# Optimization experiments

Measured on AMD Instinct MI355X. Metric: run time of the kernel, lower is better.

Reference implementation:

```python
import jax, jax.numpy as jnp
import numpy as np

B, S, D = 2, 2048, 2048
H, HK, HD = 16, 4, 128          # query heads, kv heads, head dim (H*HD == D)
HID = 4 * D                      # SwiGLU hidden (mult=4)
WIN, SINK = 1024, 4              # sliding window, attention sink tokens
EPS = 1e-6
ROPE_BASE = 10000.0


def rmsnorm(x, g):
    return x * jax.lax.rsqrt(jnp.mean(x * x, axis=-1, keepdims=True) + EPS) * g


def rope_tables(seq_len, head_dim):
    inv = 1.0 / (ROPE_BASE ** (jnp.arange(0, head_dim, 2, dtype=jnp.float32) / head_dim))
    ang = jnp.arange(seq_len, dtype=jnp.float32)[:, None] * inv[None, :]  # [S, HD/2]
    return jnp.cos(ang), jnp.sin(ang)


def apply_rope(x, cos, sin):
    # x: [B, S, h, HD]; rotate-half convention
    x1, x2 = jnp.split(x, 2, axis=-1)
    c = cos[None, :, None, :]
    s = sin[None, :, None, :]
    return jnp.concatenate([x1 * c - x2 * s, x2 * c + x1 * s], axis=-1)


def setup_inputs() -> dict:
    key = jax.random.key(0)
    ks = jax.random.split(key, 10)
    p = 0.02
    return {
        "x": jax.random.normal(ks[0], (B, S, D), dtype=jnp.float32),
        "g1": jnp.ones((D,), dtype=jnp.float32),
        "g2": jnp.ones((D,), dtype=jnp.float32),
        "wq": jax.random.normal(ks[1], (D, H * HD), dtype=jnp.float32) * p,
        "wk": jax.random.normal(ks[2], (D, HK * HD), dtype=jnp.float32) * p,
        "wv": jax.random.normal(ks[3], (D, HK * HD), dtype=jnp.float32) * p,
        "wo": jax.random.normal(ks[4], (H * HD, D), dtype=jnp.float32) * p,
        "w_gate": jax.random.normal(ks[5], (D, HID), dtype=jnp.float32) * p,
        "w_up": jax.random.normal(ks[6], (D, HID), dtype=jnp.float32) * p,
        "w_down": jax.random.normal(ks[7], (HID, D), dtype=jnp.float32) * p,
    }


def reference(x, g1, g2, wq, wk, wv, wo, w_gate, w_up, w_down):
    # ---- pre-norm attention ----
    h = rmsnorm(x, g1)
    q = (h @ wq).reshape(B, S, H, HD)
    k = (h @ wk).reshape(B, S, HK, HD)
    v = (h @ wv).reshape(B, S, HK, HD)

    cos, sin = rope_tables(S, HD)
    q = apply_rope(q, cos, sin)
    k = apply_rope(k, cos, sin)

    # GQA: expand kv heads to query heads
    rep = H // HK
    k = jnp.repeat(k, rep, axis=2)  # [B, S, H, HD]
    v = jnp.repeat(v, rep, axis=2)

    scores = jnp.einsum("bqhd,bkhd->bhqk", q, k) / jnp.sqrt(jnp.float32(HD))

    # causal + sliding-window + attention-sink mask
    i = jnp.arange(S)[:, None]
    j = jnp.arange(S)[None, :]
    allowed = (j <= i) & (((i - j) < WIN) | (j < SINK))  # [S, S]
    scores = jnp.where(allowed[None, None], scores, jnp.float32(-1e9))

    attn = jax.nn.softmax(scores, axis=-1)
    a = jnp.einsum("bhqk,bkhd->bqhd", attn, v).reshape(B, S, H * HD) @ wo

    x = x + a

    # ---- pre-norm SwiGLU FFN ----
    h2 = rmsnorm(x, g2)
    ffn = (jax.nn.silu(h2 @ w_gate) * (h2 @ w_up)) @ w_down
    return x + ffn
```

## Files before the change

kernel.cpp:

```cpp
#include <hip/hip_runtime.h>
#include <hip/hip_bf16.h>
#include <stdint.h>

#define TOK 4096
#define SEQ 2048
#define DM 2048
#define NH 16
#define NKV 4
#define HDIM 128
#define HID 8192
#define WIN 1024
#define SINKN 4

typedef float f32x4 __attribute__((ext_vector_type(4)));
typedef __bf16 bf16x8 __attribute__((ext_vector_type(8)));
typedef unsigned short u16;
typedef unsigned int u32;

#define VM(n) asm volatile("s_waitcnt vmcnt(" #n ")" ::: "memory")
#define LG(n) asm volatile("s_waitcnt lgkmcnt(" #n ")" ::: "memory")
#define SCHED0 __builtin_amdgcn_sched_barrier(0)

__device__ __forceinline__ u16 f2bf(float f) {
  union { float f; u32 u; } v; v.f = f;
  return (u16)((v.u + 0x7fffu + ((v.u >> 16) & 1u)) >> 16);
}
__device__ __forceinline__ float bf2f(u16 h) {
  union { u32 u; float f; } v; v.u = ((u32)h) << 16;
  return v.f;
}
__device__ __forceinline__ f32x4 mfma16(bf16x8 a, bf16x8 b, f32x4 c) {
  return __builtin_amdgcn_mfma_f32_16x16x32_bf16(a, b, c, 0, 0, 0);
}
__device__ __forceinline__ void gld16(const u16* g, u16* l) {
  __builtin_amdgcn_global_load_lds(
      (const __attribute__((address_space(1))) u32*)g,
      (__attribute__((address_space(3))) u32*)l, 16, 0, 0);
}
__device__ __forceinline__ void bar() {
  asm volatile("s_barrier" ::: "memory");
}
__device__ __forceinline__ void swz_rc(int c, int& row, int& k8) {
  row = 2 * (c >> 3) + (((c >> 2) & 1) ^ ((c >> 4) & 1));
  k8 = (c & 3) ^ (row & 3);
}
__device__ __forceinline__ void raster8(int wg, int nwg, int nbx, int& bx, int& by) {
  int cpx = nwg >> 3;
  int s = (wg & 7) * cpx + (wg >> 3);
  by = 8 * (s / (8 * nbx)) + (s & 7);
  bx = (s >> 3) % nbx;
}

__global__ __launch_bounds__(256)
void wtrans(const float* __restrict__ in, u16* __restrict__ out, int K, int N)
{
  __shared__ float t[32][33];
  int tx = threadIdx.x & 31, ty = threadIdx.x >> 5;
  int bx = blockIdx.x, by = blockIdx.y;
  #pragma unroll
  for (int i = 0; i < 4; i++) {
    int r = ty + i * 8;
    t[r][tx] = in[(size_t)(by * 32 + r) * N + bx * 32 + tx];
  }
  __syncthreads();
  #pragma unroll
  for (int i = 0; i < 4; i++) {
    int r = ty + i * 8;
    out[(size_t)(bx * 32 + r) * K + by * 32 + tx] = f2bf(t[tx][r]);
  }
}

__global__ __launch_bounds__(256)
void vtrans(const u16* __restrict__ in, int ld, u16* __restrict__ out)
{
  __shared__ u16 t[32][33];
  int tx = threadIdx.x & 31, ty = threadIdx.x >> 5;
  int bx = blockIdx.x;
  int by = blockIdx.y;
  #pragma unroll
  for (int i = 0; i < 4; i++) {
    int r = ty + i * 8;
    t[r][tx] = in[(size_t)(by * 32 + r) * ld + bx * 32 + tx];
  }
  __syncthreads();
  int b = (by * 32) >> 11;
  int s0 = (by * 32) & (SEQ - 1);
  #pragma unroll
  for (int i = 0; i < 4; i++) {
    int c = bx * 32 + ty + i * 8;
    out[(size_t)(b * (NKV * HDIM) + c) * SEQ + s0 + tx] = t[tx][ty + i * 8];
  }
}

__global__ __launch_bounds__(256)
void rope_table_k(float* __restrict__ ct, float* __restrict__ st)
{
  int idx = blockIdx.x * 256 + threadIdx.x;
  int pos = idx >> 6, d = idx & 63;
  float inv = powf(10000.0f, -(float)d / 64.0f);
  float a = (float)pos * inv;
  ct[idx] = cosf(a);
  st[idx] = sinf(a);
}

__global__ void rope_apply_k(u16* __restrict__ q, int ld,
                             const float* __restrict__ ct,
                             const float* __restrict__ st, float scale)
{
  int t = blockIdx.x;
  int hh = threadIdx.x >> 6;
  int d = threadIdx.x & 63;
  int pos = t & (SEQ - 1);
  size_t base = (size_t)t * ld + hh * HDIM + d;
  float x1 = bf2f(q[base]), x2 = bf2f(q[base + 64]);
  float c = ct[pos * 64 + d], s = st[pos * 64 + d];
  q[base]      = f2bf((x1 * c - x2 * s) * scale);
  q[base + 64] = f2bf((x2 * c + x1 * s) * scale);
}

__global__ __launch_bounds__(256)
void rmsnorm_k(const float* __restrict__ x, const float* __restrict__ g,
               u16* __restrict__ o)
{
  int row = blockIdx.x;
  int tid = threadIdx.x;
  const float* xr = x + (size_t)row * DM;
  float4 v0 = *(const float4*)(xr + tid * 8);
  float4 v1 = *(const float4*)(xr + tid * 8 + 4);
  float ss = v0.x*v0.x + v0.y*v0.y + v0.z*v0.z + v0.w*v0.w
           + v1.x*v1.x + v1.y*v1.y + v1.z*v1.z + v1.w*v1.w;
  #pragma unroll
  for (int d = 1; d < 64; d <<= 1) ss += __shfl_xor(ss, d);
  __shared__ float red[4];
  if ((tid & 63) == 0) red[tid >> 6] = ss;
  __syncthreads();
  float inv = rsqrtf((red[0] + red[1] + red[2] + red[3]) * (1.0f / DM) + 1e-6f);
  float4 g0 = *(const float4*)(g + tid * 8);
  float4 g1 = *(const float4*)(g + tid * 8 + 4);
  ushort4 o0, o1;
  o0.x = f2bf(v0.x * inv * g0.x); o0.y = f2bf(v0.y * inv * g0.y);
  o0.z = f2bf(v0.z * inv * g0.z); o0.w = f2bf(v0.w * inv * g0.w);
  o1.x = f2bf(v1.x * inv * g1.x); o1.y = f2bf(v1.y * inv * g1.y);
  o1.z = f2bf(v1.z * inv * g1.z); o1.w = f2bf(v1.w * inv * g1.w);
  *(ushort4*)(o + (size_t)row * DM + tid * 8) = o0;
  *(ushort4*)(o + (size_t)row * DM + tid * 8 + 4) = o1;
}

template<int EPI>
__global__ __launch_bounds__(512, 1)
void gemmp(const u16* __restrict__ A, const u16* __restrict__ Bt,
           u16* __restrict__ Cb, float* __restrict__ Cf,
           const float* __restrict__ X, int M, int N, int K, int nbx)
{
  constexpr int ASZ = 128 * 64;
  constexpr int SLOT = ASZ + 256 * 64;
  __shared__ u16 lds[3 * SLOT];

  int bx, by;
  raster8(blockIdx.x, gridDim.x, nbx, bx, by);
  int m0 = by * 128;
  int n0 = bx * 256;

  int tid = threadIdx.x;
  int l = tid & 63, w = tid >> 6;
  int l16 = l & 15, lg = l >> 4;
  int wr = w >> 2, wc = w & 3;

  int aoff[4][2], boff[4][2];
  #pragma unroll
  for (int m = 0; m < 4; m++)
    #pragma unroll
    for (int kk = 0; kk < 2; kk++) {
      int row = wr * 64 + m * 16 + l16;
      aoff[m][kk] = ((row * 128 + kk * 64 + lg * 16) ^ ((row & 7) << 4)) >> 1;
    }
  #pragma unroll
  for (int n = 0; n < 4; n++)
    #pragma unroll
    for (int kk = 0; kk < 2; kk++) {
      int br = wc * 64 + n * 16 + l16;
      boff[n][kk] = ASZ + (((br * 128 + kk * 64 + lg * 16) ^ ((br & 7) << 4)) >> 1);
    }

  int urow = tid >> 3;
  int cc = (tid & 7) ^ (urow & 7);
  const u16* pA[2];
  const u16* pB[4];
  pA[0] = A + (size_t)(m0 + urow) * K + cc * 8;
  pA[1] = A + (size_t)(m0 + 64 + urow) * K + cc * 8;
  #pragma unroll
  for (int u = 0; u < 4; u++)
    pB[u] = Bt + (size_t)(n0 + u * 64 + urow) * K + cc * 8;

  const int NT = K >> 6;

  auto stA = [&](int tt, int u) {
    gld16(pA[u] + (size_t)tt * 64, lds + (tt % 3) * SLOT + u * 4096 + tid * 8);
  };
  auto stB = [&](int tt, int u) {
    gld16(pB[u] + (size_t)tt * 64, lds + (tt % 3) * SLOT + ASZ + u * 4096 + tid * 8);
  };

  #pragma unroll
  for (int u = 0; u < 4; u++) stB(0, u);
  stA(0, 0); stA(0, 1);
  #pragma unroll
  for (int u = 0; u < 4; u++) stB(1, u);
  stA(1, 0); stA(1, 1);
  VM(6);
  bar();

  f32x4 acc[4][4];
  f32x4 zero = {0.f, 0.f, 0.f, 0.f};
  #pragma unroll
  for (int m = 0; m < 4; m++)
    #pragma unroll
    for (int n = 0; n < 4; n++) acc[m][n] = zero;

  for (int t = 0; t < NT; ++t) {
    u16* cur = lds + (t % 3) * SLOT;
    const bool st = (t + 2 < NT);

    if (st) { stB(t + 2, 0); stB(t + 2, 1); stB(t + 2, 2); }
    bf16x8 a[4][2], b[2][2], c2[2][2];
    #pragma unroll
    for (int m = 0; m < 4; m++) {
      a[m][0] = *(const bf16x8*)(cur + aoff[m][0]);
      a[m][1] = *(const bf16x8*)(cur + aoff[m][1]);
    }
    #pragma unroll
    for (int n = 0; n < 2; n++) {
      b[n][0] = *(const bf16x8*)(cur + boff[n][0]);
      b[n][1] = *(const bf16x8*)(cur + boff[n][1]);
    }
    SCHED0;
    #pragma unroll
    for (int n = 0; n < 2; n++) {
      c2[n][0] = *(const bf16x8*)(cur + boff[n + 2][0]);
      c2[n][1] = *(const bf16x8*)(cur + boff[n + 2][1]);
    }
    bar();
    LG(4);
    SCHED0;
    __builtin_amdgcn_s_setprio(1);
    #pragma unroll
    for (int m = 0; m < 4; m++)
      #pragma unroll
      for (int n = 0; n < 2; n++) {
        acc[m][n] = mfma16(a[m][0], b[n][0], acc[m][n]);
        acc[m][n] = mfma16(a[m][1], b[n][1], acc[m][n]);
      }
    __builtin_amdgcn_s_setprio(0);
    SCHED0;
    bar();

    if (st) { stB(t + 2, 3); stA(t + 2, 0); stA(t + 2, 1); }
    if (st) { VM(6); }
    else if (t + 1 < NT) { VM(0); }
    bar();
    LG(0);
    SCHED0;
    __builtin_amdgcn_s_setprio(1);
    #pragma unroll
    for (int m = 0; m < 4; m++)
      #pragma unroll
      for (int n = 0; n < 2; n++) {
        acc[m][n + 2] = mfma16(a[m][0], c2[n][0], acc[m][n + 2]);
        acc[m][n + 2] = mfma16(a[m][1], c2[n][1], acc[m][n + 2]);
      }
    __builtin_amdgcn_s_setprio(0);
    SCHED0;
    bar();
  }

  #pragma unroll
  for (int m = 0; m < 4; m++) {
    int row = m0 + wr * 64 + m * 16 + lg * 4;
    #pragma unroll
    for (int n = 0; n < 4; n++) {
      int col = n0 + wc * 64 + n * 16 + l16;
      #pragma unroll
      for (int r = 0; r < 4; r++) {
        size_t idx = (size_t)(row + r) * N + col;
        float v = acc[m][n][r];
        if (EPI == 0) {
          Cb[idx] = f2bf(v);
        } else if (EPI == 1) {
          Cf[idx] = X[idx] + v;
        } else {
          Cf[idx] += v;
        }
      }
    }
  }
}

template<int EPI, int GU, int SPLITK>
__global__ __launch_bounds__(512, 1)
void gemm256(const u16* __restrict__ A, const u16* __restrict__ B1,
             const u16* __restrict__ B2, u16* __restrict__ Cb,
             float* __restrict__ Cf, int Kst, int NT, int N, int nbx)
{
  constexpr int SLOT = 32768;
  __shared__ u16 lds[2 * SLOT];

  int wg = blockIdx.x;
  int nwg = gridDim.x;
  int kh = 0;
  if (SPLITK) { int half = nwg >> 1; kh = (wg >= half); wg -= kh * half; nwg = half; }
  int bx, by;
  raster8(wg, nwg, nbx, bx, by);
  int m0 = by * 256;
  int n0 = bx * (GU ? 128 : 256);
  size_t k0 = (size_t)kh * NT * 64;

  int tid = threadIdx.x;
  int l = tid & 63, w = tid >> 6;
  int l16 = l & 15, lg = l >> 4;
  int wr = w >> 2, wc = w & 3;

  int aoff[4][2], boff[2][2];
  #pragma unroll
  for (int mm = 0; mm < 4; mm++)
    #pragma unroll
    for (int kk = 0; kk < 2; kk++) {
      int ar = wr * 64 + mm * 16 + l16;
      aoff[mm][kk] = ((ar * 128 + ((kk * 64 + lg * 16) ^ ((ar & 7) << 4))) >> 1);
    }
  #pragma unroll
  for (int nn = 0; nn < 2; nn++)
    #pragma unroll
    for (int kk = 0; kk < 2; kk++) {
      int br = wc * 32 + nn * 16 + l16;
      boff[nn][kk] = 16384 + ((br * 128 + ((kk * 64 + lg * 16) ^ ((br & 7) << 4))) >> 1);
    }

  int rh = tid >> 3;
  int cc = (tid & 7) ^ (rh & 7);
  const u16* pA[4];
  #pragma unroll
  for (int u = 0; u < 4; u++)
    pA[u] = A + (size_t)(m0 + u * 64 + rh) * Kst + k0 + cc * 8;
  const u16* pB[4];
  #pragma unroll
  for (int u = 0; u < 4; u++) {
    if (GU) pB[u] = (u < 2 ? B1 + (size_t)(n0 + u * 64 + rh) * Kst
                           : B2 + (size_t)(n0 + (u - 2) * 64 + rh) * Kst) + k0 + cc * 8;
    else    pB[u] = B1 + (size_t)(n0 + u * 64 + rh) * Kst + k0 + cc * 8;
  }

  auto stA = [&](int tt, int h) {
    u16* d = lds + (tt & 1) * SLOT + h * 8192;
    gld16(pA[h * 2 + 0] + (size_t)tt * 64, d + tid * 8);
    gld16(pA[h * 2 + 1] + (size_t)tt * 64, d + 4096 + tid * 8);
  };
  auto stB = [&](int tt, int h) {
    u16* d = lds + (tt & 1) * SLOT + 16384 + h * 8192;
    gld16(pB[h * 2 + 0] + (size_t)tt * 64, d + tid * 8);
    gld16(pB[h * 2 + 1] + (size_t)tt * 64, d + 4096 + tid * 8);
  };

  stA(0, 0); stB(0, 0); stA(0, 1); stB(0, 1);
  stA(1, 0); stB(1, 0); stA(1, 1);
  VM(6);
  bar();

  f32x4 acc[8][4];
  f32x4 zero = {0.f, 0.f, 0.f, 0.f};
  #pragma unroll
  for (int m = 0; m < 8; m++)
    #pragma unroll
    for (int n = 0; n < 4; n++) acc[m][n] = zero;

  for (int t = 0; t < NT; ++t) {
    u16* cur = lds + (t & 1) * SLOT;
    bf16x8 a0[4][2], a1[4][2], b0[2][2], b1[2][2];

    #pragma unroll
    for (int mm = 0; mm < 4; mm++)
      #pragma unroll
      for (int kk = 0; kk < 2; kk++)
        a0[mm][kk] = *(const bf16x8*)(cur + aoff[mm][kk]);
    #pragma unroll
    for (int nn = 0; nn < 2; nn++)
      #pragma unroll
      for (int kk = 0; kk < 2; kk++)
        b0[nn][kk] = *(const bf16x8*)(cur + boff[nn][kk]);
    if (t + 1 < NT) stB(t + 1, 1);
    LG(8);
    bar();
    LG(0);
    SCHED0;
    __builtin_amdgcn_s_setprio(1);
    #pragma unroll
    for (int mm = 0; mm < 4; mm++)
      #pragma unroll
      for (int nn = 0; nn < 2; nn++)
        #pragma unroll
        for (int kk = 0; kk < 2; kk++)
          acc[mm][nn] = mfma16(a0[mm][kk], b0[nn][kk], acc[mm][nn]);
    __builtin_amdgcn_s_setprio(0);
    SCHED0;
    bar();

    #pragma unroll
    for (int nn = 0; nn < 2; nn++)
      #pragma unroll
      for (int kk = 0; kk < 2; kk++)
        b1[nn][kk] = *(const bf16x8*)(cur + boff[nn][kk] + 8192);
    if (t + 2 < NT) stA(t + 2, 0);
    bar();
    LG(0);
    SCHED0;
    __builtin_amdgcn_s_setprio(1);
    #pragma unroll
    for (int mm = 0; mm < 4; mm++)
      #pragma unroll
      for (int nn = 0; nn < 2; nn++)
        #pragma unroll
        for (int kk = 0; kk < 2; kk++)
          acc[mm][2 + nn] = mfma16(a0[mm][kk], b1[nn][kk], acc[mm][2 + nn]);
    __builtin_amdgcn_s_setprio(0);
    SCHED0;
    bar();

    #pragma unroll
    for (int mm = 0; mm < 4; mm++)
      #pragma unroll
      for (int kk = 0; kk < 2; kk++)
        a1[mm][kk] = *(const bf16x8*)(cur + aoff[mm][kk] + 8192);
    if (t + 2 < NT) stB(t + 2, 0);
    bar();
    LG(0);
    SCHED0;
    __builtin_amdgcn_s_setprio(1);
    #pragma unroll
    for (int mm = 0; mm < 4; mm++)
      #pragma unroll
      for (int nn = 0; nn < 2; nn++)
        #pragma unroll
        for (int kk = 0; kk < 2; kk++)
          acc[4 + mm][nn] = mfma16(a1[mm][kk], b0[nn][kk], acc[4 + mm][nn]);
    __builtin_amdgcn_s_setprio(0);
    SCHED0;
    bar();

    if (t + 2 < NT) { stA(t + 2, 1); VM(6); }
    else if (t + 1 < NT) { VM(0); }
    bar();
    SCHED0;
    __builtin_amdgcn_s_setprio(1);
    #pragma unroll
    for (int mm = 0; mm < 4; mm++)
      #pragma unroll
      for (int nn = 0; nn < 2; nn++)
        #pragma unroll
        for (int kk = 0; kk < 2; kk++)
          acc[4 + mm][2 + nn] = mfma16(a1[mm][kk], b1[nn][kk], acc[4 + mm][2 + nn]);
    __builtin_amdgcn_s_setprio(0);
    SCHED0;
    bar();
  }

  if (GU) {
    #pragma unroll
    for (int m = 0; m < 8; m++) {
      int row = m0 + (m >> 2) * 128 + wr * 64 + (m & 3) * 16 + lg * 4;
      #pragma unroll
      for (int nn = 0; nn < 2; nn++) {
        int col = n0 + wc * 32 + nn * 16 + l16;
        #pragma unroll
        for (int r = 0; r < 4; r++) {
          float gt = acc[m][nn][r];
          float up = acc[m][2 + nn][r];
          float sg = gt / (1.0f + __expf(-gt));
          Cb[(size_t)(row + r) * N + col] = f2bf(sg * up);
        }
      }
    }
  } else {
    #pragma unroll
    for (int m = 0; m < 8; m++) {
      int row = m0 + (m >> 2) * 128 + wr * 64 + (m & 3) * 16 + lg * 4;
      #pragma unroll
      for (int n = 0; n < 4; n++) {
        int col = n0 + (n >> 1) * 128 + wc * 32 + (n & 1) * 16 + l16;
        #pragma unroll
        for (int r = 0; r < 4; r++) {
          size_t idx = (size_t)(row + r) * N + col;
          if (EPI == 0) Cb[idx] = f2bf(acc[m][n][r]);
          else          atomicAdd(Cf + idx, acc[m][n][r]);
        }
      }
    }
  }
}

__global__ __launch_bounds__(256)
void attn_k(const u16* __restrict__ qb, int ldq,
            const u16* __restrict__ kb, int ldk,
            const u16* __restrict__ vbt, u16* __restrict__ ao)
{
  int q0 = blockIdx.x * 128;
  int h = blockIdx.y;
  int b = blockIdx.z;
  int hk = h >> 2;
  int tid = threadIdx.x;
  int w = tid >> 6, l = tid & 63;
  int l16 = l & 15, lg = l >> 4;

  __shared__ u16 Ks[32 * 128];
  __shared__ u16 Vt[128 * 32];
  __shared__ u16 Ps[4][32 * 40];
  u16* Pw = Ps[w];

  bf16x8 qf[2][4];
  #pragma unroll
  for (int m = 0; m < 2; m++)
    #pragma unroll
    for (int kd = 0; kd < 4; kd++) {
      int row = q0 + w * 32 + m * 16 + l16;
      qf[m][kd] = *(const bf16x8*)(qb + (size_t)(b * SEQ + row) * ldq
                                   + h * HDIM + kd * 32 + lg * 8);
    }

  f32x4 oacc[2][8];
  float mrun[2][4], lrun[2][4];
  f32x4 zero = {0.f, 0.f, 0.f, 0.f};
  #pragma unroll
  for (int m = 0; m < 2; m++) {
    #pragma unroll
    for (int nd = 0; nd < 8; nd++) oacc[m][nd] = zero;
    #pragma unroll
    for (int r = 0; r < 4; r++) { mrun[m][r] = -1e9f; lrun[m][r] = 0.f; }
  }

  int kr0 = tid >> 4,        kc0 = (tid & 15) ^ (kr0 & 7);
  int kr1 = (tid + 256) >> 4, kc1 = (tid & 15) ^ (kr1 & 7);
  int vd0, vk0, vd1, vk1;
  swz_rc(tid, vd0, vk0);
  swz_rc(tid + 256, vd1, vk1);
  const u16* kbase = kb + (size_t)(b * SEQ) * ldk + hk * HDIM;
  const u16* vbase = vbt + (size_t)(b * NKV + hk) * HDIM * SEQ;

  int koff[2][4];
  #pragma unroll
  for (int n = 0; n < 2; n++)
    #pragma unroll
    for (int kd = 0; kd < 4; kd++) {
      int key = n * 16 + l16;
      koff[n][kd] = ((key * 128) + kd * 32 + lg * 8) ^ ((key & 7) * 8);
    }
  int voff[8];
  #pragma unroll
  for (int nd = 0; nd < 8; nd++) {
    int d = nd * 16 + l16;
    voff[nd] = (d * 32 + lg * 8) ^ ((d & 7) * 8);
  }

  int lo = (q0 >= WIN) ? ((q0 - (WIN - 1)) >> 5) : 0;
  int hi = (q0 + 127) >> 5;

  for (int it = (lo > 0 ? lo - 1 : 0); it <= hi; ++it) {
    int kt = (it < lo) ? 0 : it;
    gld16(kbase + (size_t)(kt * 32 + kr0) * ldk + kc0 * 8, Ks + tid * 8);
    gld16(kbase + (size_t)(kt * 32 + kr1) * ldk + kc1 * 8, Ks + (tid + 256) * 8);
    gld16(vbase + (size_t)vd0 * SEQ + kt * 32 + vk0 * 8, Vt + tid * 8);
    gld16(vbase + (size_t)vd1 * SEQ + kt * 32 + vk1 * 8, Vt + (tid + 256) * 8);
    __syncthreads();

    f32x4 sacc[2][2];
    sacc[0][0] = zero; sacc[0][1] = zero; sacc[1][0] = zero; sacc[1][1] = zero;
    #pragma unroll
    for (int kd = 0; kd < 4; kd++) {
      bf16x8 kf0 = *(const bf16x8*)(Ks + koff[0][kd]);
      bf16x8 kf1 = *(const bf16x8*)(Ks + koff[1][kd]);
      #pragma unroll
      for (int m = 0; m < 2; m++) {
        sacc[m][0] = mfma16(qf[m][kd], kf0, sacc[m][0]);
        sacc[m][1] = mfma16(qf[m][kd], kf1, sacc[m][1]);
      }
    }

    #pragma unroll
    for (int m = 0; m < 2; m++) {
      float sc[4];
      #pragma unroll
      for (int r = 0; r < 4; r++) {
        int i = q0 + w * 32 + m * 16 + lg * 4 + r;
        int j0 = kt * 32 + l16;
        int j1 = j0 + 16;
        float s0 = sacc[m][0][r];
        float s1 = sacc[m][1][r];
        bool ok0 = (j0 <= i) && ((i - j0 < WIN) || (j0 < SINKN));
        bool ok1 = (j1 <= i) && ((i - j1 < WIN) || (j1 < SINKN));
        s0 = ok0 ? s0 : -1e9f;
        s1 = ok1 ? s1 : -1e9f;
        float mx = fmaxf(s0, s1);
        mx = fmaxf(mx, __shfl_xor(mx, 1));
        mx = fmaxf(mx, __shfl_xor(mx, 2));
        mx = fmaxf(mx, __shfl_xor(mx, 4));
        mx = fmaxf(mx, __shfl_xor(mx, 8));
        float mold = mrun[m][r];
        float mnew = fmaxf(mold, mx);
        float scl = __expf(mold - mnew);
        mrun[m][r] = mnew;
        float p0 = __expf(s0 - mnew);
        float p1 = __expf(s1 - mnew);
        int prow = m * 16 + lg * 4 + r;
        Pw[prow * 40 + l16] = f2bf(p0);
        Pw[prow * 40 + 16 + l16] = f2bf(p1);
        float ps = p0 + p1;
        ps += __shfl_xor(ps, 1);
        ps += __shfl_xor(ps, 2);
        ps += __shfl_xor(ps, 4);
        ps += __shfl_xor(ps, 8);
        lrun[m][r] = lrun[m][r] * scl + ps;
        sc[r] = scl;
      }
      #pragma unroll
      for (int nd = 0; nd < 8; nd++) {
        oacc[m][nd][0] *= sc[0];
        oacc[m][nd][1] *= sc[1];
        oacc[m][nd][2] *= sc[2];
        oacc[m][nd][3] *= sc[3];
      }
    }

    bf16x8 pa0 = *(const bf16x8*)(Pw + l16 * 40 + lg * 8);
    bf16x8 pa1 = *(const bf16x8*)(Pw + (16 + l16) * 40 + lg * 8);
    #pragma unroll
    for (int nd = 0; nd < 8; nd++) {
      bf16x8 vf = *(const bf16x8*)(Vt + voff[nd]);
      oacc[0][nd] = mfma16(pa0, vf, oacc[0][nd]);
      oacc[1][nd] = mfma16(pa1, vf, oacc[1][nd]);
    }
    __syncthreads();
  }

  #pragma unroll
  for (int m = 0; m < 2; m++)
    #pragma unroll
    for (int r = 0; r < 4; r++) {
      float invl = 1.0f / lrun[m][r];
      int row = q0 + w * 32 + m * 16 + lg * 4 + r;
      #pragma unroll
      for (int nd = 0; nd < 8; nd++) {
        int col = nd * 16 + l16;
        ao[(size_t)(b * SEQ + row) * (NH * HDIM) + h * HDIM + col] =
            f2bf(oacc[m][nd][r] * invl);
      }
    }
}

extern "C" void kernel_launch(void* const* d_in, const int* in_sizes, int n_in,
                              void* d_out, int out_size, void* d_ws, size_t ws_size,
                              hipStream_t stream)
{
  (void)in_sizes; (void)n_in; (void)out_size;
  const float* x  = (const float*)d_in[0];
  const float* g1 = (const float*)d_in[1];
  const float* g2 = (const float*)d_in[2];
  const float* wq = (const float*)d_in[3];
  const float* wk = (const float*)d_in[4];
  const float* wv = (const float*)d_in[5];
  const float* wo = (const float*)d_in[6];
  const float* wg = (const float*)d_in[7];
  const float* wu = (const float*)d_in[8];
  const float* wd = (const float*)d_in[9];
  float* out = (float*)d_out;

  char* ws = (char*)d_ws;
  size_t off = 0;
  auto alloc = [&](size_t bytes) {
    char* p = ws + off;
    off += (bytes + 255) & ~(size_t)255;
    return p;
  };
  const int NQKV = 3072;
  u16* wqkv_t = (u16*)alloc((size_t)NQKV * DM * 2);
  u16* wo_t   = (u16*)alloc((size_t)DM * DM * 2);
  u16* wg_t   = (u16*)alloc((size_t)HID * DM * 2);
  u16* wu_t   = (u16*)alloc((size_t)HID * DM * 2);
  u16* wd_t   = (u16*)alloc((size_t)DM * HID * 2);
  u16* hb     = (u16*)alloc((size_t)TOK * DM * 2);
  char* span0 = ws + off;
  u16* qkvb   = (u16*)alloc((size_t)TOK * NQKV * 2);
  u16* vbt    = (u16*)alloc((size_t)TOK * NKV * HDIM * 2);
  u16* aob    = (u16*)alloc((size_t)TOK * NH * HDIM * 2);
  size_t span_used = (size_t)(ws + off - span0);
  size_t gu_need = (size_t)TOK * HID * 2;
  if (gu_need > span_used) alloc(gu_need - span_used);
  u16* gu = (u16*)span0;
  float* ct  = (float*)alloc((size_t)SEQ * 64 * 4);
  float* st  = (float*)alloc((size_t)SEQ * 64 * 4);
  if (off > ws_size) return;

  dim3 blk(256);
  dim3 blk512(512);

  wtrans<<<dim3(DM / 32, DM / 32), blk, 0, stream>>>(wq, wqkv_t, DM, DM);
  wtrans<<<dim3((NKV * HDIM) / 32, DM / 32), blk, 0, stream>>>(wk, wqkv_t + (size_t)DM * DM, DM, NKV * HDIM);
  wtrans<<<dim3((NKV * HDIM) / 32, DM / 32), blk, 0, stream>>>(wv, wqkv_t + (size_t)(DM + NKV * HDIM) * DM, DM, NKV * HDIM);
  wtrans<<<dim3(DM / 32, DM / 32), blk, 0, stream>>>(wo, wo_t, DM, DM);
  wtrans<<<dim3(HID / 32, DM / 32), blk, 0, stream>>>(wg, wg_t, DM, HID);
  wtrans<<<dim3(HID / 32, DM / 32), blk, 0, stream>>>(wu, wu_t, DM, HID);
  wtrans<<<dim3(DM / 32, HID / 32), blk, 0, stream>>>(wd, wd_t, HID, DM);

  rope_table_k<<<SEQ * 64 / 256, blk, 0, stream>>>(ct, st);
  rmsnorm_k<<<TOK, blk, 0, stream>>>(x, g1, hb);

  gemm256<0, 0, 0><<<dim3((NQKV / 256) * (TOK / 256)), blk512, 0, stream>>>(
      hb, wqkv_t, nullptr, qkvb, nullptr, DM, DM / 64, NQKV, NQKV / 256);

  rope_apply_k<<<TOK, dim3(NH * 64), 0, stream>>>(qkvb, NQKV, ct, st, 0.08838834764831845f);
  rope_apply_k<<<TOK, dim3(NKV * 64), 0, stream>>>(qkvb + DM, NQKV, ct, st, 1.0f);
  vtrans<<<dim3((NKV * HDIM) / 32, TOK / 32), blk, 0, stream>>>(qkvb + DM + NKV * HDIM, NQKV, vbt);

  attn_k<<<dim3(SEQ / 128, NH, 2), blk, 0, stream>>>(qkvb, NQKV, qkvb + DM, NQKV, vbt, aob);

  gemmp<1><<<dim3((DM / 256) * (TOK / 128)), blk512, 0, stream>>>(
      aob, wo_t, nullptr, out, x, TOK, DM, DM, DM / 256);
  rmsnorm_k<<<TOK, blk, 0, stream>>>(out, g2, hb);

  gemm256<0, 1, 0><<<dim3((HID / 128) * (TOK / 256)), blk512, 0, stream>>>(
      hb, wg_t, wu_t, gu, nullptr, DM, DM / 64, HID, HID / 128);

  gemm256<4, 0, 1><<<dim3(2 * (DM / 256) * (TOK / 256)), blk512, 0, stream>>>(
      gu, wd_t, nullptr, nullptr, out, HID, HID / 128, DM, DM / 256);
}
```

Before: 770.9 us.

## Merge weight transposes, double-buffer attention K/V, split-K the output projection

Merges the seven weight-transpose launches into one kernel that picks its source and destination from the block index. The attention kernel now double-buffers the K/V tiles with async loads, so the next tile's global load overlaps the current tile's compute. The output projection moves from the dedicated gemmp kernel to the split-K gemm256 path with an accumulate epilogue. The residual x is copied into out during the first rmsnorm so the split-K atomic adds accumulate onto it. It also adds unroll 2 to the gemm256 main loop, and the split-K accumulation order may make results nondeterministic.

```diff
diff --git a/kernel.cpp b/kernel.cpp
--- a/kernel.cpp
+++ b/kernel.cpp
@@ -52,21 +52,38 @@
 }
 
 __global__ __launch_bounds__(256)
-void wtrans(const float* __restrict__ in, u16* __restrict__ out, int K, int N)
-{
+void wtrans_all(const float* __restrict__ wq, const float* __restrict__ wk,
+                const float* __restrict__ wv, const float* __restrict__ wo,
+                const float* __restrict__ wg, const float* __restrict__ wu,
+                const float* __restrict__ wd,
+                u16* __restrict__ dqkv, u16* __restrict__ dwo,
+                u16* __restrict__ dwg, u16* __restrict__ dwu,
+                u16* __restrict__ dwd)
+{
+  int id = blockIdx.x;
+  const float* src; u16* dst; int K, N, lgn;
+  if (id < 4096)       { src = wq; dst = dqkv;                        K = 2048; N = 2048; lgn = 6; }
+  else if (id < 5120)  { id -= 4096;  src = wk; dst = dqkv + (size_t)DM * DM;          K = 2048; N = 512;  lgn = 4; }
+  else if (id < 6144)  { id -= 5120;  src = wv; dst = dqkv + (size_t)(DM + 512) * DM;  K = 2048; N = 512;  lgn = 4; }
+  else if (id < 10240) { id -= 6144;  src = wo; dst = dwo;            K = 2048; N = 2048; lgn = 6; }
+  else if (id < 26624) { id -= 10240; src = wg; dst = dwg;            K = 2048; N = 8192; lgn = 8; }
+  else if (id < 43008) { id -= 26624; src = wu; dst = dwu;            K = 2048; N = 8192; lgn = 8; }
+  else                 { id -= 43008; src = wd; dst = dwd;            K = 8192; N = 2048; lgn = 6; }
+  int bx = id & ((1 << lgn) - 1);
+  int by = id >> lgn;
+
   __shared__ float t[32][33];
   int tx = threadIdx.x & 31, ty = threadIdx.x >> 5;
-  int bx = blockIdx.x, by = blockIdx.y;
   #pragma unroll
   for (int i = 0; i < 4; i++) {
     int r = ty + i * 8;
-    t[r][tx] = in[(size_t)(by * 32 + r) * N + bx * 32 + tx];
+    t[r][tx] = src[(size_t)(by * 32 + r) * N + bx * 32 + tx];
   }
   __syncthreads();
   #pragma unroll
   for (int i = 0; i < 4; i++) {
     int r = ty + i * 8;
-    out[(size_t)(bx * 32 + r) * K + by * 32 + tx] = f2bf(t[tx][r]);
+    dst[(size_t)(bx * 32 + r) * K + by * 32 + tx] = f2bf(t[tx][r]);
   }
 }
 
@@ -120,7 +137,7 @@
 
 __global__ __launch_bounds__(256)
 void rmsnorm_k(const float* __restrict__ x, const float* __restrict__ g,
-               u16* __restrict__ o)
+               u16* __restrict__ o, float* __restrict__ xcopy)
 {
   int row = blockIdx.x;
   int tid = threadIdx.x;
@@ -135,6 +152,10 @@
   if ((tid & 63) == 0) red[tid >> 6] = ss;
   __syncthreads();
   float inv = rsqrtf((red[0] + red[1] + red[2] + red[3]) * (1.0f / DM) + 1e-6f);
+  if (xcopy) {
+    *(float4*)(xcopy + (size_t)row * DM + tid * 8) = v0;
+    *(float4*)(xcopy + (size_t)row * DM + tid * 8 + 4) = v1;
+  }
   float4 g0 = *(const float4*)(g + tid * 8);
   float4 g1 = *(const float4*)(g + tid * 8 + 4);
   ushort4 o0, o1;
@@ -144,155 +165,6 @@
   o1.z = f2bf(v1.z * inv * g1.z); o1.w = f2bf(v1.w * inv * g1.w);
   *(ushort4*)(o + (size_t)row * DM + tid * 8) = o0;
   *(ushort4*)(o + (size_t)row * DM + tid * 8 + 4) = o1;
-}
-
-template<int EPI>
-__global__ __launch_bounds__(512, 1)
-void gemmp(const u16* __restrict__ A, const u16* __restrict__ Bt,
-           u16* __restrict__ Cb, float* __restrict__ Cf,
-           const float* __restrict__ X, int M, int N, int K, int nbx)
-{
-  constexpr int ASZ = 128 * 64;
-  constexpr int SLOT = ASZ + 256 * 64;
-  __shared__ u16 lds[3 * SLOT];
-
-  int bx, by;
-  raster8(blockIdx.x, gridDim.x, nbx, bx, by);
-  int m0 = by * 128;
-  int n0 = bx * 256;
-
-  int tid = threadIdx.x;
-  int l = tid & 63, w = tid >> 6;
-  int l16 = l & 15, lg = l >> 4;
-  int wr = w >> 2, wc = w & 3;
-
-  int aoff[4][2], boff[4][2];
-  #pragma unroll
-  for (int m = 0; m < 4; m++)
-    #pragma unroll
-    for (int kk = 0; kk < 2; kk++) {
-      int row = wr * 64 + m * 16 + l16;
-      aoff[m][kk] = ((row * 128 + kk * 64 + lg * 16) ^ ((row & 7) << 4)) >> 1;
-    }
-  #pragma unroll
-  for (int n = 0; n < 4; n++)
-    #pragma unroll
-    for (int kk = 0; kk < 2; kk++) {
-      int br = wc * 64 + n * 16 + l16;
-      boff[n][kk] = ASZ + (((br * 128 + kk * 64 + lg * 16) ^ ((br & 7) << 4)) >> 1);
-    }
-
-  int urow = tid >> 3;
-  int cc = (tid & 7) ^ (urow & 7);
-  const u16* pA[2];
-  const u16* pB[4];
-  pA[0] = A + (size_t)(m0 + urow) * K + cc * 8;
-  pA[1] = A + (size_t)(m0 + 64 + urow) * K + cc * 8;
-  #pragma unroll
-  for (int u = 0; u < 4; u++)
-    pB[u] = Bt + (size_t)(n0 + u * 64 + urow) * K + cc * 8;
-
-  const int NT = K >> 6;
-
-  auto stA = [&](int tt, int u) {
-    gld16(pA[u] + (size_t)tt * 64, lds + (tt % 3) * SLOT + u * 4096 + tid * 8);
-  };
-  auto stB = [&](int tt, int u) {
-    gld16(pB[u] + (size_t)tt * 64, lds + (tt % 3) * SLOT + ASZ + u * 4096 + tid * 8);
-  };
-
-  #pragma unroll
-  for (int u = 0; u < 4; u++) stB(0, u);
-  stA(0, 0); stA(0, 1);
-  #pragma unroll
-  for (int u = 0; u < 4; u++) stB(1, u);
-  stA(1, 0); stA(1, 1);
-  VM(6);
-  bar();
-
-  f32x4 acc[4][4];
-  f32x4 zero = {0.f, 0.f, 0.f, 0.f};
-  #pragma unroll
-  for (int m = 0; m < 4; m++)
-    #pragma unroll
-    for (int n = 0; n < 4; n++) acc[m][n] = zero;
-
-  for (int t = 0; t < NT; ++t) {
-    u16* cur = lds + (t % 3) * SLOT;
-    const bool st = (t + 2 < NT);
-
-    if (st) { stB(t + 2, 0); stB(t + 2, 1); stB(t + 2, 2); }
-    bf16x8 a[4][2], b[2][2], c2[2][2];
-    #pragma unroll
-    for (int m = 0; m < 4; m++) {
-      a[m][0] = *(const bf16x8*)(cur + aoff[m][0]);
-      a[m][1] = *(const bf16x8*)(cur + aoff[m][1]);
-    }
-    #pragma unroll
-    for (int n = 0; n < 2; n++) {
-      b[n][0] = *(const bf16x8*)(cur + boff[n][0]);
-      b[n][1] = *(const bf16x8*)(cur + boff[n][1]);
-    }
-    SCHED0;
-    #pragma unroll
-    for (int n = 0; n < 2; n++) {
-      c2[n][0] = *(const bf16x8*)(cur + boff[n + 2][0]);
-      c2[n][1] = *(const bf16x8*)(cur + boff[n + 2][1]);
-    }
-    bar();
-    LG(4);
-    SCHED0;
-    __builtin_amdgcn_s_setprio(1);
-    #pragma unroll
-    for (int m = 0; m < 4; m++)
-      #pragma unroll
-      for (int n = 0; n < 2; n++) {
-        acc[m][n] = mfma16(a[m][0], b[n][0], acc[m][n]);
-        acc[m][n] = mfma16(a[m][1], b[n][1], acc[m][n]);
-      }
-    __builtin_amdgcn_s_setprio(0);
-    SCHED0;
-    bar();
-
-    if (st) { stB(t + 2, 3); stA(t + 2, 0); stA(t + 2, 1); }
-    if (st) { VM(6); }
-    else if (t + 1 < NT) { VM(0); }
-    bar();
-    LG(0);
-    SCHED0;
-    __builtin_amdgcn_s_setprio(1);
-    #pragma unroll
-    for (int m = 0; m < 4; m++)
-      #pragma unroll
-      for (int n = 0; n < 2; n++) {
-        acc[m][n + 2] = mfma16(a[m][0], c2[n][0], acc[m][n + 2]);
-        acc[m][n + 2] = mfma16(a[m][1], c2[n][1], acc[m][n + 2]);
-      }
-    __builtin_amdgcn_s_setprio(0);
-    SCHED0;
-    bar();
-  }
-
-  #pragma unroll
-  for (int m = 0; m < 4; m++) {
-    int row = m0 + wr * 64 + m * 16 + lg * 4;
-    #pragma unroll
-    for (int n = 0; n < 4; n++) {
-      int col = n0 + wc * 64 + n * 16 + l16;
-      #pragma unroll
-      for (int r = 0; r < 4; r++) {
-        size_t idx = (size_t)(row + r) * N + col;
-        float v = acc[m][n][r];
-        if (EPI == 0) {
-          Cb[idx] = f2bf(v);
-        } else if (EPI == 1) {
-          Cf[idx] = X[idx] + v;
-        } else {
-          Cf[idx] += v;
-        }
-      }
-    }
-  }
 }
 
 template<int EPI, int GU, int SPLITK>
@@ -372,6 +244,7 @@
     #pragma unroll
     for (int n = 0; n < 4; n++) acc[m][n] = zero;
 
+  #pragma unroll 2
   for (int t = 0; t < NT; ++t) {
     u16* cur = lds + (t & 1) * SLOT;
     bf16x8 a0[4][2], a1[4][2], b0[2][2], b1[2][2];
@@ -509,8 +382,8 @@
   int w = tid >> 6, l = tid & 63;
   int l16 = l & 15, lg = l >> 4;
 
-  __shared__ u16 Ks[32 * 128];
-  __shared__ u16 Vt[128 * 32];
+  __shared__ u16 Ks[2][32 * 128];
+  __shared__ u16 Vt[2][128 * 32];
   __shared__ u16 Ps[4][32 * 40];
   u16* Pw = Ps[w];
 
@@ -558,23 +431,34 @@
     voff[nd] = (d * 32 + lg * 8) ^ ((d & 7) * 8);
   }
 
+  auto stage = [&](int kt, int bsel) {
+    gld16(kbase + (size_t)(kt * 32 + kr0) * ldk + kc0 * 8, Ks[bsel] + tid * 8);
+    gld16(kbase + (size_t)(kt * 32 + kr1) * ldk + kc1 * 8, Ks[bsel] + (tid + 256) * 8);
+    gld16(vbase + (size_t)vd0 * SEQ + kt * 32 + vk0 * 8, Vt[bsel] + tid * 8);
+    gld16(vbase + (size_t)vd1 * SEQ + kt * 32 + vk1 * 8, Vt[bsel] + (tid + 256) * 8);
+  };
+
   int lo = (q0 >= WIN) ? ((q0 - (WIN - 1)) >> 5) : 0;
   int hi = (q0 + 127) >> 5;
-
-  for (int it = (lo > 0 ? lo - 1 : 0); it <= hi; ++it) {
+  int it0 = (lo > 0 ? lo - 1 : 0);
+
+  stage((it0 < lo) ? 0 : it0, 0);
+  int bsel = 0;
+
+  for (int it = it0; it <= hi; ++it) {
     int kt = (it < lo) ? 0 : it;
-    gld16(kbase + (size_t)(kt * 32 + kr0) * ldk + kc0 * 8, Ks + tid * 8);
-    gld16(kbase + (size_t)(kt * 32 + kr1) * ldk + kc1 * 8, Ks + (tid + 256) * 8);
-    gld16(vbase + (size_t)vd0 * SEQ + kt * 32 + vk0 * 8, Vt + tid * 8);
-    gld16(vbase + (size_t)vd1 * SEQ + kt * 32 + vk1 * 8, Vt + (tid + 256) * 8);
-    __syncthreads();
+    if (it < hi) { stage(it + 1, bsel ^ 1); VM(4); }
+    else         { VM(0); }
+    bar();
+    const u16* Ksb = Ks[bsel];
+    const u16* Vtb = Vt[bsel];
 
     f32x4 sacc[2][2];
     sacc[0][0] = zero; sacc[0][1] = zero; sacc[1][0] = zero; sacc[1][1] = zero;
     #pragma unroll
     for (int kd = 0; kd < 4; kd++) {
-      bf16x8 kf0 = *(const bf16x8*)(Ks + koff[0][kd]);
-      bf16x8 kf1 = *(const bf16x8*)(Ks + koff[1][kd]);
+      bf16x8 kf0 = *(const bf16x8*)(Ksb + koff[0][kd]);
+      bf16x8 kf1 = *(const bf16x8*)(Ksb + koff[1][kd]);
       #pragma unroll
       for (int m = 0; m < 2; m++) {
         sacc[m][0] = mfma16(qf[m][kd], kf0, sacc[m][0]);
@@ -631,11 +515,12 @@
     bf16x8 pa1 = *(const bf16x8*)(Pw + (16 + l16) * 40 + lg * 8);
     #pragma unroll
     for (int nd = 0; nd < 8; nd++) {
-      bf16x8 vf = *(const bf16x8*)(Vt + voff[nd]);
+      bf16x8 vf = *(const bf16x8*)(Vtb + voff[nd]);
       oacc[0][nd] = mfma16(pa0, vf, oacc[0][nd]);
       oacc[1][nd] = mfma16(pa1, vf, oacc[1][nd]);
     }
-    __syncthreads();
+    bar();
+    bsel ^= 1;
   }
 
   #pragma unroll
@@ -699,16 +584,11 @@
   dim3 blk(256);
   dim3 blk512(512);
 
-  wtrans<<<dim3(DM / 32, DM / 32), blk, 0, stream>>>(wq, wqkv_t, DM, DM);
-  wtrans<<<dim3((NKV * HDIM) / 32, DM / 32), blk, 0, stream>>>(wk, wqkv_t + (size_t)DM * DM, DM, NKV * HDIM);
-  wtrans<<<dim3((NKV * HDIM) / 32, DM / 32), blk, 0, stream>>>(wv, wqkv_t + (size_t)(DM + NKV * HDIM) * DM, DM, NKV * HDIM);
-  wtrans<<<dim3(DM / 32, DM / 32), blk, 0, stream>>>(wo, wo_t, DM, DM);
-  wtrans<<<dim3(HID / 32, DM / 32), blk, 0, stream>>>(wg, wg_t, DM, HID);
-  wtrans<<<dim3(HID / 32, DM / 32), blk, 0, stream>>>(wu, wu_t, DM, HID);
-  wtrans<<<dim3(DM / 32, HID / 32), blk, 0, stream>>>(wd, wd_t, HID, DM);
+  wtrans_all<<<dim3(59392), blk, 0, stream>>>(wq, wk, wv, wo, wg, wu, wd,
+                                              wqkv_t, wo_t, wg_t, wu_t, wd_t);
 
   rope_table_k<<<SEQ * 64 / 256, blk, 0, stream>>>(ct, st);
-  rmsnorm_k<<<TOK, blk, 0, stream>>>(x, g1, hb);
+  rmsnorm_k<<<TOK, blk, 0, stream>>>(x, g1, hb, out);
 
   gemm256<0, 0, 0><<<dim3((NQKV / 256) * (TOK / 256)), blk512, 0, stream>>>(
       hb, wqkv_t, nullptr, qkvb, nullptr, DM, DM / 64, NQKV, NQKV / 256);
@@ -719,9 +599,10 @@
 
   attn_k<<<dim3(SEQ / 128, NH, 2), blk, 0, stream>>>(qkvb, NQKV, qkvb + DM, NQKV, vbt, aob);
 
-  gemmp<1><<<dim3((DM / 256) * (TOK / 128)), blk512, 0, stream>>>(
-      aob, wo_t, nullptr, out, x, TOK, DM, DM, DM / 256);
-  rmsnorm_k<<<TOK, blk, 0, stream>>>(out, g2, hb);
+  gemm256<4, 0, 1><<<dim3(2 * (DM / 256) * (TOK / 256)), blk512, 0, stream>>>(
+      aob, wo_t, nullptr, nullptr, out, DM, DM / 128, DM, DM / 256);
+
+  rmsnorm_k<<<TOK, blk, 0, stream>>>(out, g2, hb, nullptr);
 
   gemm256<0, 1, 0><<<dim3((HID / 128) * (TOK / 256)), blk512, 0, stream>>>(
       hb, wg_t, wu_t, gu, nullptr, DM, DM / 64, HID, HID / 128);
```

Measured after the change: 804.4 us. +4.4%, slower.

## Merge weight transposes, fuse Q RoPE into attention, double-buffer KV tiles

Applied to the files above, without the earlier changes.

Collapses seven weight-transpose launches into one kernel that picks its source matrix from the block index. Q RoPE and scaling are now applied inside the attention kernel when Q fragments are loaded, which removes a separate pass over Q. The attention K/V tiles are double-buffered in LDS so the next tile's loads overlap the current tile's compute. A GEMM main loop also gets an unroll-2 hint. The costs are more LDS per attention block, with a possible occupancy hit, an extra bf16 rounding step on Q, and more registers from the unroll.

```diff
diff --git a/kernel.cpp b/kernel.cpp
--- a/kernel.cpp
+++ b/kernel.cpp
@@ -52,21 +52,38 @@
 }
 
 __global__ __launch_bounds__(256)
-void wtrans(const float* __restrict__ in, u16* __restrict__ out, int K, int N)
-{
+void wtrans_all(const float* __restrict__ wq, const float* __restrict__ wk,
+                const float* __restrict__ wv, const float* __restrict__ wo,
+                const float* __restrict__ wg, const float* __restrict__ wu,
+                const float* __restrict__ wd,
+                u16* __restrict__ dqkv, u16* __restrict__ dwo,
+                u16* __restrict__ dwg, u16* __restrict__ dwu,
+                u16* __restrict__ dwd)
+{
+  int id = blockIdx.x;
+  const float* src; u16* dst; int K, N, lgn;
+  if (id < 4096)       { src = wq; dst = dqkv;                        K = 2048; N = 2048; lgn = 6; }
+  else if (id < 5120)  { id -= 4096;  src = wk; dst = dqkv + (size_t)DM * DM;          K = 2048; N = 512;  lgn = 4; }
+  else if (id < 6144)  { id -= 5120;  src = wv; dst = dqkv + (size_t)(DM + 512) * DM;  K = 2048; N = 512;  lgn = 4; }
+  else if (id < 10240) { id -= 6144;  src = wo; dst = dwo;            K = 2048; N = 2048; lgn = 6; }
+  else if (id < 26624) { id -= 10240; src = wg; dst = dwg;            K = 2048; N = 8192; lgn = 8; }
+  else if (id < 43008) { id -= 26624; src = wu; dst = dwu;            K = 2048; N = 8192; lgn = 8; }
+  else                 { id -= 43008; src = wd; dst = dwd;            K = 8192; N = 2048; lgn = 6; }
+  int bx = id & ((1 << lgn) - 1);
+  int by = id >> lgn;
+
   __shared__ float t[32][33];
   int tx = threadIdx.x & 31, ty = threadIdx.x >> 5;
-  int bx = blockIdx.x, by = blockIdx.y;
   #pragma unroll
   for (int i = 0; i < 4; i++) {
     int r = ty + i * 8;
-    t[r][tx] = in[(size_t)(by * 32 + r) * N + bx * 32 + tx];
+    t[r][tx] = src[(size_t)(by * 32 + r) * N + bx * 32 + tx];
   }
   __syncthreads();
   #pragma unroll
   for (int i = 0; i < 4; i++) {
     int r = ty + i * 8;
-    out[(size_t)(bx * 32 + r) * K + by * 32 + tx] = f2bf(t[tx][r]);
+    dst[(size_t)(bx * 32 + r) * K + by * 32 + tx] = f2bf(t[tx][r]);
   }
 }
 
@@ -372,6 +389,7 @@
     #pragma unroll
     for (int n = 0; n < 4; n++) acc[m][n] = zero;
 
+  #pragma unroll 2
   for (int t = 0; t < NT; ++t) {
     u16* cur = lds + (t & 1) * SLOT;
     bf16x8 a0[4][2], a1[4][2], b0[2][2], b1[2][2];
@@ -499,7 +517,8 @@
 __global__ __launch_bounds__(256)
 void attn_k(const u16* __restrict__ qb, int ldq,
             const u16* __restrict__ kb, int ldk,
-            const u16* __restrict__ vbt, u16* __restrict__ ao)
+            const u16* __restrict__ vbt, u16* __restrict__ ao,
+            const float* __restrict__ ct, const float* __restrict__ st)
 {
   int q0 = blockIdx.x * 128;
   int h = blockIdx.y;
@@ -509,20 +528,36 @@
   int w = tid >> 6, l = tid & 63;
   int l16 = l & 15, lg = l >> 4;
 
-  __shared__ u16 Ks[32 * 128];
-  __shared__ u16 Vt[128 * 32];
+  __shared__ u16 Ks[2][32 * 128];
+  __shared__ u16 Vt[2][128 * 32];
   __shared__ u16 Ps[4][32 * 40];
   u16* Pw = Ps[w];
 
+  const float qscale = 0.08838834764831845f;
   bf16x8 qf[2][4];
   #pragma unroll
-  for (int m = 0; m < 2; m++)
-    #pragma unroll
-    for (int kd = 0; kd < 4; kd++) {
-      int row = q0 + w * 32 + m * 16 + l16;
+  for (int m = 0; m < 2; m++) {
+    int row = q0 + w * 32 + m * 16 + l16;
+    #pragma unroll
+    for (int kd = 0; kd < 4; kd++)
       qf[m][kd] = *(const bf16x8*)(qb + (size_t)(b * SEQ + row) * ldq
                                    + h * HDIM + kd * 32 + lg * 8);
-    }
+    const float* ctp = ct + (size_t)row * 64;
+    const float* stp = st + (size_t)row * 64;
+    #pragma unroll
+    for (int pr = 0; pr < 2; pr++) {
+      bf16x8 lo = qf[m][pr], hi = qf[m][pr + 2];
+      int dl = pr * 32 + lg * 8;
+      #pragma unroll
+      for (int j = 0; j < 8; j++) {
+        float c = ctp[dl + j], s = stp[dl + j];
+        float x1 = (float)lo[j], x2 = (float)hi[j];
+        lo[j] = (__bf16)((x1 * c - x2 * s) * qscale);
+        hi[j] = (__bf16)((x2 * c + x1 * s) * qscale);
+      }
+      qf[m][pr] = lo; qf[m][pr + 2] = hi;
+    }
+  }
 
   f32x4 oacc[2][8];
   float mrun[2][4], lrun[2][4];
@@ -558,23 +593,34 @@
     voff[nd] = (d * 32 + lg * 8) ^ ((d & 7) * 8);
   }
 
+  auto stage = [&](int kt, int bsel) {
+    gld16(kbase + (size_t)(kt * 32 + kr0) * ldk + kc0 * 8, Ks[bsel] + tid * 8);
+    gld16(kbase + (size_t)(kt * 32 + kr1) * ldk + kc1 * 8, Ks[bsel] + (tid + 256) * 8);
+    gld16(vbase + (size_t)vd0 * SEQ + kt * 32 + vk0 * 8, Vt[bsel] + tid * 8);
+    gld16(vbase + (size_t)vd1 * SEQ + kt * 32 + vk1 * 8, Vt[bsel] + (tid + 256) * 8);
+  };
+
   int lo = (q0 >= WIN) ? ((q0 - (WIN - 1)) >> 5) : 0;
   int hi = (q0 + 127) >> 5;
-
-  for (int it = (lo > 0 ? lo - 1 : 0); it <= hi; ++it) {
+  int it0 = (lo > 0 ? lo - 1 : 0);
+
+  stage((it0 < lo) ? 0 : it0, 0);
+  int bsel = 0;
+
+  for (int it = it0; it <= hi; ++it) {
     int kt = (it < lo) ? 0 : it;
-    gld16(kbase + (size_t)(kt * 32 + kr0) * ldk + kc0 * 8, Ks + tid * 8);
-    gld16(kbase + (size_t)(kt * 32 + kr1) * ldk + kc1 * 8, Ks + (tid + 256) * 8);
-    gld16(vbase + (size_t)vd0 * SEQ + kt * 32 + vk0 * 8, Vt + tid * 8);
-    gld16(vbase + (size_t)vd1 * SEQ + kt * 32 + vk1 * 8, Vt + (tid + 256) * 8);
-    __syncthreads();
+    if (it < hi) { stage(it + 1, bsel ^ 1); VM(4); }
+    else         { VM(0); }
+    bar();
+    const u16* Ksb = Ks[bsel];
+    const u16* Vtb = Vt[bsel];
 
     f32x4 sacc[2][2];
     sacc[0][0] = zero; sacc[0][1] = zero; sacc[1][0] = zero; sacc[1][1] = zero;
     #pragma unroll
     for (int kd = 0; kd < 4; kd++) {
-      bf16x8 kf0 = *(const bf16x8*)(Ks + koff[0][kd]);
-      bf16x8 kf1 = *(const bf16x8*)(Ks + koff[1][kd]);
+      bf16x8 kf0 = *(const bf16x8*)(Ksb + koff[0][kd]);
+      bf16x8 kf1 = *(const bf16x8*)(Ksb + koff[1][kd]);
       #pragma unroll
       for (int m = 0; m < 2; m++) {
         sacc[m][0] = mfma16(qf[m][kd], kf0, sacc[m][0]);
@@ -631,11 +677,12 @@
     bf16x8 pa1 = *(const bf16x8*)(Pw + (16 + l16) * 40 + lg * 8);
     #pragma unroll
     for (int nd = 0; nd < 8; nd++) {
-      bf16x8 vf = *(const bf16x8*)(Vt + voff[nd]);
+      bf16x8 vf = *(const bf16x8*)(Vtb + voff[nd]);
       oacc[0][nd] = mfma16(pa0, vf, oacc[0][nd]);
       oacc[1][nd] = mfma16(pa1, vf, oacc[1][nd]);
     }
-    __syncthreads();
+    bar();
+    bsel ^= 1;
   }
 
   #pragma unroll
@@ -699,13 +746,8 @@
   dim3 blk(256);
   dim3 blk512(512);
 
-  wtrans<<<dim3(DM / 32, DM / 32), blk, 0, stream>>>(wq, wqkv_t, DM, DM);
-  wtrans<<<dim3((NKV * HDIM) / 32, DM / 32), blk, 0, stream>>>(wk, wqkv_t + (size_t)DM * DM, DM, NKV * HDIM);
-  wtrans<<<dim3((NKV * HDIM) / 32, DM / 32), blk, 0, stream>>>(wv, wqkv_t + (size_t)(DM + NKV * HDIM) * DM, DM, NKV * HDIM);
-  wtrans<<<dim3(DM / 32, DM / 32), blk, 0, stream>>>(wo, wo_t, DM, DM);
-  wtrans<<<dim3(HID / 32, DM / 32), blk, 0, stream>>>(wg, wg_t, DM, HID);
-  wtrans<<<dim3(HID / 32, DM / 32), blk, 0, stream>>>(wu, wu_t, DM, HID);
-  wtrans<<<dim3(DM / 32, HID / 32), blk, 0, stream>>>(wd, wd_t, HID, DM);
+  wtrans_all<<<dim3(59392), blk, 0, stream>>>(wq, wk, wv, wo, wg, wu, wd,
+                                              wqkv_t, wo_t, wg_t, wu_t, wd_t);
 
   rope_table_k<<<SEQ * 64 / 256, blk, 0, stream>>>(ct, st);
   rmsnorm_k<<<TOK, blk, 0, stream>>>(x, g1, hb);
@@ -713,11 +755,10 @@
   gemm256<0, 0, 0><<<dim3((NQKV / 256) * (TOK / 256)), blk512, 0, stream>>>(
       hb, wqkv_t, nullptr, qkvb, nullptr, DM, DM / 64, NQKV, NQKV / 256);
 
-  rope_apply_k<<<TOK, dim3(NH * 64), 0, stream>>>(qkvb, NQKV, ct, st, 0.08838834764831845f);
   rope_apply_k<<<TOK, dim3(NKV * 64), 0, stream>>>(qkvb + DM, NQKV, ct, st, 1.0f);
   vtrans<<<dim3((NKV * HDIM) / 32, TOK / 32), blk, 0, stream>>>(qkvb + DM + NKV * HDIM, NQKV, vbt);
 
-  attn_k<<<dim3(SEQ / 128, NH, 2), blk, 0, stream>>>(qkvb, NQKV, qkvb + DM, NQKV, vbt, aob);
+  attn_k<<<dim3(SEQ / 128, NH, 2), blk, 0, stream>>>(qkvb, NQKV, qkvb + DM, NQKV, vbt, aob, ct, st);
 
   gemmp<1><<<dim3((DM / 256) * (TOK / 128)), blk512, 0, stream>>>(
       aob, wo_t, nullptr, out, x, TOK, DM, DM, DM / 256);
```

After: 736.8 us (median of 3 runs). -4.4%, faster.
